# Kernel optimization log

Hardware: AMD Instinct MI355X
Metric: run time of the kernel (lower is better)

## Reference

```python
import jax, jax.numpy as jnp
import numpy as np

B, N = 1, 1024
VOCAB = 32000
DIM = 512
DEPTH = 2
HEADS = 8
DIM_HEAD = 64
DIM_INNER = HEADS * DIM_HEAD      # 512
DIM_FF = 4 * DIM                  # 2048
MAX_SEQ = 1024
EPS = 1e-12


def sq_dist(x, w):
    # squared L2 distance between rows of x [..., d] and rows of w [m, d] -> [..., m]
    xs = jnp.sum(x * x, axis=-1, keepdims=True)
    ws = jnp.sum(w * w, axis=-1)
    return xs - 2.0 * jnp.einsum('...d,md->...m', x, w) + ws


def cdist(x, w):
    # euclidean distance (torch.cdist equivalent)
    return jnp.sqrt(jnp.maximum(sq_dist(x, w), 0.0))


def rmsnorm(x, gamma):
    # F.normalize(x, dim=-1) * sqrt(dim) * (gamma + 1)
    n = jnp.linalg.norm(x, axis=-1, keepdims=True)
    return x / jnp.maximum(n, EPS) * (DIM ** 0.5) * (gamma + 1.0)


def attention(x, qkv_w, out_w):
    b, n, _ = x.shape
    qkv = cdist(x, qkv_w)                                   # [b, n, 3*inner] (to_qkv: squared=False)
    qkv = qkv.reshape(b, n, 3, HEADS, DIM_HEAD)
    qkv = qkv.transpose(2, 0, 3, 1, 4)                      # [3, b, h, n, d]
    q, k, v = qkv[0], qkv[1], qkv[2]
    qs = jnp.sum(q * q, axis=-1)                            # [b, h, n]
    ks = jnp.sum(k * k, axis=-1)                            # [b, h, n]
    # -||q_i - k_j||^2 = 2 q.k - ||q||^2 - ||k||^2
    sim = (2.0 * jnp.einsum('bhid,bhjd->bhij', q, k)
           - qs[..., :, None] - ks[..., None, :]) * (DIM_HEAD ** -0.5)
    attn = jax.nn.softmax(sim, axis=-1)
    o = jnp.einsum('bhij,bhjd->bhid', attn, v)
    o = o.transpose(0, 2, 1, 3).reshape(b, n, DIM_INNER)    # merge heads
    return o @ out_w.T                                      # plain Linear, no bias


def feedforward(x, w_in, b_in, w_out):
    h = -sq_dist(x, w_in) + b_in                            # proj_in: squared=True, negate=True, bias
    h = jax.nn.gelu(h, approximate=False)
    return h @ w_out.T                                      # plain Linear, no bias


def setup_inputs() -> dict:
    key = jax.random.key(0)
    ks = jax.random.split(key, 12)
    nrm = lambda k, s: jax.random.normal(k, s, dtype=jnp.float32)
    return {
        'tokens': jax.random.randint(ks[0], (B, N), 0, VOCAB),
        'token_emb': nrm(ks[1], (VOCAB, DIM)),
        'pos_emb': nrm(ks[2], (MAX_SEQ, DIM)),
        'qkv_w': nrm(ks[3], (DEPTH, 3 * DIM_INNER, DIM)),
        'attn_out_w': nrm(ks[4], (DEPTH, DIM, DIM_INNER)) * 0.02,
        'ff_in_w': nrm(ks[5], (DEPTH, DIM_FF, DIM)),
        'ff_in_b': nrm(ks[6], (DEPTH, DIM_FF)),
        'ff_out_w': nrm(ks[7], (DEPTH, DIM, DIM_FF)) * 0.02,
        'attn_gamma': jnp.zeros((DEPTH, DIM), jnp.float32),
        'ff_gamma': jnp.zeros((DEPTH, DIM), jnp.float32),
        'final_gamma': jnp.zeros((DIM,), jnp.float32),
    }


def reference(tokens, token_emb, pos_emb, qkv_w, attn_out_w, ff_in_w, ff_in_b,
              ff_out_w, attn_gamma, ff_gamma, final_gamma):
    n = tokens.shape[-1]
    x = token_emb[tokens] + pos_emb[:n]                     # [b, n, dim]
    for l in range(DEPTH):
        x = attention(rmsnorm(x, attn_gamma[l]), qkv_w[l], attn_out_w[l]) + x
        x = feedforward(rmsnorm(x, ff_gamma[l]), ff_in_w[l], ff_in_b[l], ff_out_w[l]) + x
    x = rmsnorm(x, final_gamma)
    return -sq_dist(x, token_emb)                           # [b, n, vocab] logits
```

## Files before the change

kernel.cpp:

```cpp
#include <hip/hip_runtime.h>
#include <math.h>

#define DIMM  512
#define NSEQ  1024
#define NHEAD 8
#define DH    64
#define DFF   2048
#define NVOC  32000
#define NDEPTH 2
#define VCENTER 32.0f
#define KVB   64
#define QBLK  32
#define QKOFF ((size_t)NHEAD * NSEQ * DH)
#define FLASH_BLOCKS (NSEQ / QBLK * NHEAD)
#define CONV_ROWS_PER_LAYER (NVOC / NDEPTH)
#define CONV_BLOCKS (CONV_ROWS_PER_LAYER / 64)
#define WCONV_PER_LAYER (3 * DIMM + DIMM + DFF + DIMM)

typedef __attribute__((ext_vector_type(8))) __bf16 bf16x8;
typedef __attribute__((ext_vector_type(4))) __bf16 bf16x4;
typedef __attribute__((ext_vector_type(4))) float f32x4;

__device__ __forceinline__ void g2l16(const void* g, void* l) {
    __builtin_amdgcn_global_load_lds(
        (const __attribute__((address_space(1))) void*)g,
        (__attribute__((address_space(3))) void*)l, 16, 0, 0);
}

#define WAITV(N) asm volatile("s_waitcnt vmcnt(" #N ")" ::: "memory")

template<int NTHR>
__device__ __forceinline__ void conv_weight_row(
    int bid, int l,
    const float* __restrict__ qkv_w, const float* __restrict__ attn_out_w,
    const float* __restrict__ ff_in_w, const float* __restrict__ ff_out_w,
    __bf16* __restrict__ wq16, __bf16* __restrict__ wa16,
    __bf16* __restrict__ wfi16, __bf16* __restrict__ wfo16,
    float* __restrict__ wsq_qkv, float* __restrict__ wsq_ff, float* red) {
    const int tid = threadIdx.x;
    const float* src; __bf16* dst; float* ssq; int K = DIMM; int row;
    if (bid < 3 * DIMM) {
        row = l * 3 * DIMM + bid; src = qkv_w; dst = wq16; ssq = wsq_qkv;
    } else if ((bid -= 3 * DIMM) < DIMM) {
        row = l * DIMM + bid; src = attn_out_w; dst = wa16; ssq = nullptr;
    } else if ((bid -= DIMM) < DFF) {
        row = l * DFF + bid; src = ff_in_w; dst = wfi16; ssq = wsq_ff;
    } else {
        bid -= DFF; row = l * DIMM + bid; src = ff_out_w; dst = wfo16; ssq = nullptr; K = DFF;
    }
    const float* s = src + (size_t)row * K;
    __bf16* d = dst + (size_t)row * K;
    float ss = 0.f;
    for (int j = tid; j < K; j += NTHR) {
        float v = s[j];
        d[j] = (__bf16)v;
        ss += v * v;
    }
    #pragma unroll
    for (int off = 32; off; off >>= 1) ss += __shfl_down(ss, off, 64);
    if ((tid & 63) == 0) red[tid >> 6] = ss;
    __syncthreads();
    if (tid == 0 && ssq) {
        float t = red[0] + red[1];
        if (NTHR == 256) t += red[2] + red[3];
        ssq[row] = t;
    }
}

__launch_bounds__(256)
__global__ void conv_embed(const float* __restrict__ qkv_w, const float* __restrict__ attn_out_w,
                           const float* __restrict__ ff_in_w, const float* __restrict__ ff_out_w,
                           __bf16* __restrict__ wq16, __bf16* __restrict__ wa16,
                           __bf16* __restrict__ wfi16, __bf16* __restrict__ wfo16,
                           float* __restrict__ wsq_qkv, float* __restrict__ wsq_ff,
                           const int* __restrict__ tokens, const float* __restrict__ temb,
                           const float* __restrict__ pemb, const float* __restrict__ gamma,
                           float* __restrict__ x, __bf16* __restrict__ y,
                           float* __restrict__ xs) {
    const int tid = threadIdx.x;
    __shared__ float red[4];

    if (blockIdx.x >= WCONV_PER_LAYER) {
        const int i = blockIdx.x - WCONV_PER_LAYER;
        int tok = tokens[i];
        const float* e = temb + (size_t)tok * DIMM;
        const float* pp = pemb + (size_t)i * DIMM;
        float v0 = e[tid] + pp[tid];
        float v1 = e[tid + 256] + pp[tid + 256];
        x[(size_t)i * DIMM + tid]       = v0;
        x[(size_t)i * DIMM + tid + 256] = v1;
        float ss = v0 * v0 + v1 * v1;
        #pragma unroll
        for (int off = 32; off; off >>= 1) ss += __shfl_down(ss, off, 64);
        if ((tid & 63) == 0) red[tid >> 6] = ss;
        __syncthreads();
        float tot = red[0] + red[1] + red[2] + red[3];
        float scale = 22.627416997969522f / fmaxf(sqrtf(tot), 1e-12f);
        float y0 = v0 * scale * (gamma[tid] + 1.0f);
        float y1 = v1 * scale * (gamma[tid + 256] + 1.0f);
        y[(size_t)i * DIMM + tid]       = (__bf16)y0;
        y[(size_t)i * DIMM + tid + 256] = (__bf16)y1;
        float s2 = y0 * y0 + y1 * y1;
        __syncthreads();
        #pragma unroll
        for (int off = 32; off; off >>= 1) s2 += __shfl_down(s2, off, 64);
        if ((tid & 63) == 0) red[tid >> 6] = s2;
        __syncthreads();
        if (tid == 0) xs[i] = red[0] + red[1] + red[2] + red[3];
        return;
    }

    conv_weight_row<256>(blockIdx.x, 0, qkv_w, attn_out_w, ff_in_w, ff_out_w,
                         wq16, wa16, wfi16, wfo16, wsq_qkv, wsq_ff, red);
}

template<int S>
__launch_bounds__(256)
__global__ void rms_red(const float* __restrict__ parts, float* __restrict__ x,
                        const float* __restrict__ gamma,
                        __bf16* __restrict__ y, float* __restrict__ xs) {
    int i = blockIdx.x;
    int tid = threadIdx.x;
    float* xr = x + (size_t)i * DIMM;
    float v0 = xr[tid], v1 = xr[tid + 256];
    #pragma unroll
    for (int s = 0; s < S; s++) {
        const float* pr = parts + (size_t)s * NSEQ * DIMM + (size_t)i * DIMM;
        v0 += pr[tid];
        v1 += pr[tid + 256];
    }
    xr[tid] = v0;
    xr[tid + 256] = v1;
    float ss = v0 * v0 + v1 * v1;
    __shared__ float red[4];
    #pragma unroll
    for (int off = 32; off; off >>= 1) ss += __shfl_down(ss, off, 64);
    if ((tid & 63) == 0) red[tid >> 6] = ss;
    __syncthreads();
    float tot = red[0] + red[1] + red[2] + red[3];
    float scale = 22.627416997969522f / fmaxf(sqrtf(tot), 1e-12f);
    float y0 = v0 * scale * (gamma[tid] + 1.0f);
    float y1 = v1 * scale * (gamma[tid + 256] + 1.0f);
    y[(size_t)i * DIMM + tid]       = (__bf16)y0;
    y[(size_t)i * DIMM + tid + 256] = (__bf16)y1;
    float s2 = y0 * y0 + y1 * y1;
    __syncthreads();
    #pragma unroll
    for (int off = 32; off; off >>= 1) s2 += __shfl_down(s2, off, 64);
    if ((tid & 63) == 0) red[tid >> 6] = s2;
    __syncthreads();
    if (tid == 0) xs[i] = red[0] + red[1] + red[2] + red[3];
}

enum { MODE_LINEAR = 0, MODE_CDIST = 1, MODE_FFGELU = 2, MODE_LOGITS = 3 };

template<int MODE>
__device__ __forceinline__ void write_elem(void* Cout, int r, int c, int M, float dot,
                                           float xsr, const float* __restrict__ ws,
                                           const float* __restrict__ bias) {
    if (MODE == MODE_LINEAR) {
        ((float*)Cout)[(size_t)r * M + c] = dot;
    } else if (MODE == MODE_FFGELU) {
        float d2 = xsr + ws[c] - 2.0f * dot;
        float hh = -d2 + bias[c];
        float v = 0.5f * hh * (1.0f + erff(hh * 0.70710678118654752f));
        ((__bf16*)Cout)[(size_t)r * M + c] = (__bf16)v;
    }
}

__launch_bounds__(512)
__global__ void gemm_logits(const __bf16* __restrict__ A, const __bf16* __restrict__ W,
                            const float* __restrict__ xs, const float* __restrict__ ws,
                            float* __restrict__ out) {
    __shared__ __align__(16) char smem[49152 + 98304];
    __bf16* As = (__bf16*)smem;
    __bf16* Bs = (__bf16*)(smem + 49152);
    float* tile = (float*)smem;
    const int tid = threadIdx.x;
    const int lane = tid & 63;
    const int wv = tid >> 6;
    const int wr = wv >> 2, wc = wv & 3;

    int id = blockIdx.x;
    id = (id & 7) * 125 + (id >> 3);
    const int row0 = (id & 7) * 128;
    const int col0 = (id >> 3) * 256;

    const int scol = ((tid & 3) ^ ((tid >> 3) & 3)) * 8;
    const __bf16* gA = A + (size_t)(row0 + (tid >> 2)) * DIMM + scol;
    const __bf16* gB = W + (size_t)(col0 + (tid >> 2)) * DIMM + scol;
    const int lrow = lane & 15;
    const int l4 = lane >> 4;
    const int slot = (l4 ^ ((lrow >> 1) & 3)) * 8;

    auto stageChunk = [&](int k0, int b) {
        g2l16(gA + k0,                      As + b * 4096 + tid * 8);
        g2l16(gB + k0,                      Bs + b * 8192 + tid * 8);
        g2l16(gB + (size_t)128 * DIMM + k0, Bs + b * 8192 + 4096 + tid * 8);
    };

    f32x4 acc[4][4] = {};
    const int nP = DIMM >> 6;
    stageChunk(0, 0);  stageChunk(32, 1);
    stageChunk(64, 2); stageChunk(96, 3);
    int pb = 0;
    for (int p = 0; p < nP; p++) {
        if (p < nP - 1) WAITV(6); else WAITV(0);
        __builtin_amdgcn_s_barrier();
        __builtin_amdgcn_sched_barrier(0);
        if (p + 2 < nP) {
            int nb = pb + 2; if (nb >= 3) nb -= 3;
            stageChunk((p + 2) << 6,        nb * 2);
            stageChunk(((p + 2) << 6) + 32, nb * 2 + 1);
        }
        #pragma unroll
        for (int half = 0; half < 2; half++) {
            const int b = pb * 2 + half;
            bf16x8 af[4], bfr[4];
            #pragma unroll
            for (int m = 0; m < 4; m++)
                af[m] = *(const bf16x8*)(As + b * 4096 + (wr * 64 + m * 16 + lrow) * 32 + slot);
            #pragma unroll
            for (int n = 0; n < 4; n++)
                bfr[n] = *(const bf16x8*)(Bs + b * 8192 + (wc * 64 + n * 16 + lrow) * 32 + slot);
            #pragma unroll
            for (int m = 0; m < 4; m++)
                #pragma unroll
                for (int n = 0; n < 4; n++)
                    acc[m][n] = __builtin_amdgcn_mfma_f32_16x16x32_bf16(af[m], bfr[n], acc[m][n], 0, 0, 0);
        }
        if (++pb == 3) pb = 0;
    }
    __syncthreads();

    #pragma unroll
    for (int m = 0; m < 4; m++)
        #pragma unroll
        for (int j = 0; j < 4; j++) {
            const int rl = wr * 64 + m * 16 + l4 * 4 + j;
            const float xsr = xs[row0 + rl];
            const int sw = ((rl >> 2) & 3) << 2;
            #pragma unroll
            for (int n = 0; n < 4; n++) {
                const int cl = wc * 64 + n * 16 + lrow;
                tile[rl * 256 + (cl ^ sw)] = -(xsr + ws[col0 + cl] - 2.0f * acc[m][n][j]);
            }
        }
    __syncthreads();

    #pragma unroll
    for (int jj = 0; jj < 16; jj++) {
        const int f = jj * 2048 + tid * 4;
        const int rr = f >> 8, cc = f & 255;
        const int sw = ((rr >> 2) & 3) << 2;
        f32x4 v = *(const f32x4*)&tile[rr * 256 + (cc ^ sw)];
        __builtin_nontemporal_store(v, (f32x4*)&out[(size_t)(row0 + rr) * NVOC + col0 + cc]);
    }
}

template<int MODE>
__launch_bounds__(256)
__global__ void gemm64(const __bf16* __restrict__ A, const __bf16* __restrict__ W,
                       const float* __restrict__ xs, const float* __restrict__ ws,
                       const float* __restrict__ bias,
                       void* __restrict__ Cout, int K, int Kstr, int M,
                       float* __restrict__ ksout) {
    __shared__ __align__(16) __bf16 As[6 * 64 * 32];
    __shared__ __align__(16) __bf16 Bs[6 * 64 * 32];
    __shared__ float ksred[2][64];
    const int tid = threadIdx.x;
    const int lane = tid & 63;
    const int wv = tid >> 6;
    const int wr = wv >> 1, wc = wv & 1;

    const int gx = gridDim.x;
    const int total = gx * gridDim.y;
    int id = blockIdx.y * gx + blockIdx.x;
    id = (id & 7) * (total >> 3) + (id >> 3);
    const int bx = id % gx;
    const int by = id / gx;
    const int row0 = by * 64;
    const int col0 = bx * 64;
    const size_t zoff = (size_t)blockIdx.z * K;
    float* Cz = (float*)Cout + (size_t)blockIdx.z * NSEQ * M;

    const int scol = (((tid & 3) ^ ((tid >> 3) & 3))) * 8;
    const __bf16* gA = A + (size_t)(row0 + (tid >> 2)) * Kstr + scol + zoff;
    const __bf16* gB = W + (size_t)(col0 + (tid >> 2)) * Kstr + scol + zoff;
    const int lrow = lane & 15;
    const int l4 = lane >> 4;
    const int slot = (l4 ^ ((lrow >> 1) & 3)) * 8;

    auto stageChunk = [&](int k0, int b) {
        g2l16(gA + k0, &As[b * 2048 + tid * 8]);
        g2l16(gB + k0, &Bs[b * 2048 + tid * 8]);
    };

    f32x4 acc[2][2] = {};
    const int nP = K >> 6;
    stageChunk(0, 0);  stageChunk(32, 1);
    stageChunk(64, 2); stageChunk(96, 3);
    int pb = 0;
    for (int p = 0; p < nP; p++) {
        if (p < nP - 1) WAITV(4); else WAITV(0);
        __builtin_amdgcn_s_barrier();
        __builtin_amdgcn_sched_barrier(0);
        if (p + 2 < nP) {
            int nb = pb + 2; if (nb >= 3) nb -= 3;
            stageChunk((p + 2) << 6,        nb * 2);
            stageChunk(((p + 2) << 6) + 32, nb * 2 + 1);
        }
        #pragma unroll
        for (int half = 0; half < 2; half++) {
            const int b = pb * 2 + half;
            bf16x8 af[2], bfr[2];
            #pragma unroll
            for (int m = 0; m < 2; m++)
                af[m] = *(const bf16x8*)&As[b * 2048 + (wr * 32 + m * 16 + lrow) * 32 + slot];
            #pragma unroll
            for (int n = 0; n < 2; n++)
                bfr[n] = *(const bf16x8*)&Bs[b * 2048 + (wc * 32 + n * 16 + lrow) * 32 + slot];
            #pragma unroll
            for (int m = 0; m < 2; m++)
                #pragma unroll
                for (int n = 0; n < 2; n++)
                    acc[m][n] = __builtin_amdgcn_mfma_f32_16x16x32_bf16(af[m], bfr[n], acc[m][n], 0, 0, 0);
        }
        if (++pb == 3) pb = 0;
    }

    const int r_base = row0 + wr * 32 + (lane >> 4) * 4;
    const int c_base = col0 + wc * 32 + (lane & 15);

    if (MODE == MODE_CDIST) {
        const int sec = col0 >> 9;
        const int h = (col0 >> 6) & 7;
        __bf16* Qc = (__bf16*)Cout;
        float pk[2][4];
        #pragma unroll
        for (int m = 0; m < 2; m++)
            #pragma unroll
            for (int j = 0; j < 4; j++) {
                const int r = r_base + m * 16 + j;
                const float xsr = xs[r];
                pk[m][j] = 0.f;
                #pragma unroll
                for (int n = 0; n < 2; n++) {
                    const int c = c_base + n * 16;
                    float d2 = xsr + ws[c] - 2.0f * acc[m][n][j];
                    float v = sqrtf(fmaxf(d2, 0.0f)) - VCENTER;
                    __bf16 bv = (__bf16)v;
                    const int d = c & 63;
                    if (sec == 0)      Qc[((size_t)h * NSEQ + r) * DH + d] = bv;
                    else if (sec == 1) Qc[QKOFF + ((size_t)h * NSEQ + r) * DH + d] = bv;
                    else               Qc[2 * QKOFF + ((size_t)h * DH + d) * NSEQ + r] = bv;
                    float fv = (float)bv;
                    pk[m][j] += fv * fv;
                }
            }
        if (sec == 1) {
            #pragma unroll
            for (int m = 0; m < 2; m++)
                #pragma unroll
                for (int j = 0; j < 4; j++) {
                    float v = pk[m][j];
                    #pragma unroll
                    for (int off = 1; off < 16; off <<= 1) v += __shfl_xor(v, off, 64);
                    if (lrow == 0) ksred[wc][wr * 32 + m * 16 + l4 * 4 + j] = v;
                }
            __syncthreads();
            if (tid < 64)
                ksout[(size_t)h * NSEQ + row0 + tid] = ksred[0][tid] + ksred[1][tid];
        }
    } else {
        #pragma unroll
        for (int m = 0; m < 2; m++)
            #pragma unroll
            for (int j = 0; j < 4; j++) {
                const int r = r_base + m * 16 + j;
                const float xsr = (MODE == MODE_LINEAR) ? 0.f : xs[r];
                #pragma unroll
                for (int n = 0; n < 2; n++)
                    write_elem<MODE>(Cz, r, c_base + n * 16, M, acc[m][n][j], xsr, ws, bias);
            }
    }
}

__launch_bounds__(128)
__global__ void flash_attn(const __bf16* __restrict__ Qc, const __bf16* __restrict__ Kc,
                           const __bf16* __restrict__ VcT, const float* __restrict__ ks,
                           __bf16* __restrict__ O,
                           const float* __restrict__ temb, __bf16* __restrict__ temb16,
                           float* __restrict__ wsq_temb, int conv_row0,
                           const float* __restrict__ qkv_w, const float* __restrict__ attn_out_w,
                           const float* __restrict__ ff_in_w, const float* __restrict__ ff_out_w,
                           __bf16* __restrict__ wq16, __bf16* __restrict__ wa16,
                           __bf16* __restrict__ wfi16, __bf16* __restrict__ wfo16,
                           float* __restrict__ wsq_qkv, float* __restrict__ wsq_ff) {
    const int tid = threadIdx.x, lane = tid & 63, wv = tid >> 6;

    if (blockIdx.x >= FLASH_BLOCKS + CONV_BLOCKS) {
        __shared__ float redc[2];
        conv_weight_row<128>(blockIdx.x - FLASH_BLOCKS - CONV_BLOCKS, 1,
                             qkv_w, attn_out_w, ff_in_w, ff_out_w,
                             wq16, wa16, wfi16, wfo16, wsq_qkv, wsq_ff, redc);
        return;
    }
    if (blockIdx.x >= FLASH_BLOCKS) {
        const int base = conv_row0 + (blockIdx.x - FLASH_BLOCKS) * 64;
        for (int it = 0; it < 32; it++) {
            const int row = base + it * 2 + wv;
            const float* src = temb + (size_t)row * DIMM;
            float4 a = ((const float4*)src)[lane];
            float4 b2 = ((const float4*)src)[lane + 64];
            float ss = a.x * a.x + a.y * a.y + a.z * a.z + a.w * a.w
                     + b2.x * b2.x + b2.y * b2.y + b2.z * b2.z + b2.w * b2.w;
            bf16x4 oa, ob;
            oa.x = (__bf16)a.x;  oa.y = (__bf16)a.y;  oa.z = (__bf16)a.z;  oa.w = (__bf16)a.w;
            ob.x = (__bf16)b2.x; ob.y = (__bf16)b2.y; ob.z = (__bf16)b2.z; ob.w = (__bf16)b2.w;
            *(bf16x4*)&temb16[(size_t)row * DIMM + lane * 4]       = oa;
            *(bf16x4*)&temb16[(size_t)row * DIMM + 256 + lane * 4] = ob;
            #pragma unroll
            for (int off = 32; off; off >>= 1) ss += __shfl_down(ss, off, 64);
            if (lane == 0) wsq_temb[row] = ss;
        }
        return;
    }

    __shared__ __align__(16) __bf16 Qs[QBLK * 64];
    __shared__ __align__(16) __bf16 Ks[2][64 * 64];
    __shared__ __align__(16) __bf16 Vs[2][64 * 64];
    __shared__ __align__(16) __bf16 Ps[2][16 * 64];
    __shared__ float kss[2][64];
    const int h = blockIdx.x >> 5, q0 = (blockIdx.x & 31) * QBLK;
    const int l15 = lane & 15, l4 = lane >> 4;

    #pragma unroll
    for (int pass = 0; pass < 2; pass++) {
        int gl = tid + pass * 128, r = gl >> 3, gs = (gl & 7) ^ (r & 7);
        g2l16(Qc + ((size_t)h * NSEQ + q0 + r) * DH + gs * 8, &Qs[gl * 8]);
    }
    auto stage = [&](int c, int buf) {
        const int kv0 = c * KVB;
        #pragma unroll
        for (int pass = 0; pass < 4; pass++) {
            int gl = tid + pass * 128, r = gl >> 3, gs = (gl & 7) ^ (r & 7);
            g2l16(Kc + ((size_t)h * NSEQ + kv0 + r) * DH + gs * 8, &Ks[buf][gl * 8]);
            g2l16(VcT + ((size_t)h * DH + r) * NSEQ + kv0 + gs * 8, &Vs[buf][gl * 8]);
        }
        if (tid < KVB) kss[buf][tid] = ks[(size_t)h * NSEQ + c * KVB + tid];
    };
    stage(0, 0);
    __syncthreads();

    bf16x8 qf[2];
    #pragma unroll
    for (int s = 0; s < 2; s++) {
        int row = wv * 16 + l15;
        int g = (l4 + 4 * s) ^ (row & 7);
        qf[s] = *(const bf16x8*)&Qs[row * 64 + g * 8];
    }

    float m_j[4], l_j[4];
    f32x4 o_[4] = {};
    #pragma unroll
    for (int j = 0; j < 4; j++) { m_j[j] = -1e30f; l_j[j] = 0.f; }

    for (int c = 0; c < NSEQ / KVB; c++) {
        const int b = c & 1;
        if (c + 1 < NSEQ / KVB) stage(c + 1, b ^ 1);

        f32x4 sa[4] = {};
        #pragma unroll
        for (int s = 0; s < 2; s++) {
            bf16x8 kf[4];
            #pragma unroll
            for (int n = 0; n < 4; n++) {
                int row = n * 16 + l15;
                int g = (l4 + 4 * s) ^ (row & 7);
                kf[n] = *(const bf16x8*)&Ks[b][row * 64 + g * 8];
            }
            #pragma unroll
            for (int n = 0; n < 4; n++)
                sa[n] = __builtin_amdgcn_mfma_f32_16x16x32_bf16(qf[s], kf[n], sa[n], 0, 0, 0);
        }
        float ksv[4];
        #pragma unroll
        for (int n = 0; n < 4; n++) ksv[n] = kss[b][n * 16 + l15];

        float scale[4];
        #pragma unroll
        for (int j = 0; j < 4; j++) {
            float mx = -1e30f;
            #pragma unroll
            for (int n = 0; n < 4; n++) {
                float sv = sa[n][j] * 0.25f - ksv[n] * 0.125f;
                sa[n][j] = sv;
                mx = fmaxf(mx, sv);
            }
            #pragma unroll
            for (int off = 1; off < 16; off <<= 1) mx = fmaxf(mx, __shfl_xor(mx, off, 64));
            float mn = fmaxf(m_j[j], mx);
            scale[j] = expf(m_j[j] - mn);
            m_j[j] = mn;
        }
        #pragma unroll
        for (int j = 0; j < 4; j++) {
            const int row = l4 * 4 + j;
            float ls = 0.f;
            #pragma unroll
            for (int n = 0; n < 4; n++) {
                float pv = expf(sa[n][j] - m_j[j]);
                ls += pv;
                int col = n * 16 + l15;
                Ps[wv][row * 64 + ((((col >> 3) ^ (row & 7)) << 3) | (col & 7))] = (__bf16)pv;
            }
            #pragma unroll
            for (int off = 1; off < 16; off <<= 1) ls += __shfl_xor(ls, off, 64);
            l_j[j] = l_j[j] * scale[j] + ls;
            o_[0][j] *= scale[j]; o_[1][j] *= scale[j];
            o_[2][j] *= scale[j]; o_[3][j] *= scale[j];
        }

        #pragma unroll
        for (int s = 0; s < 2; s++) {
            int g = (l4 + 4 * s) ^ (l15 & 7);
            bf16x8 pf = *(const bf16x8*)&Ps[wv][l15 * 64 + g * 8];
            #pragma unroll
            for (int n = 0; n < 4; n++) {
                int row = n * 16 + l15;
                int gv = (l4 + 4 * s) ^ (row & 7);
                bf16x8 vf = *(const bf16x8*)&Vs[b][row * 64 + gv * 8];
                o_[n] = __builtin_amdgcn_mfma_f32_16x16x32_bf16(pf, vf, o_[n], 0, 0, 0);
            }
        }
        __syncthreads();
    }

    #pragma unroll
    for (int n = 0; n < 4; n++)
        #pragma unroll
        for (int j = 0; j < 4; j++) {
            int row = q0 + wv * 16 + l4 * 4 + j;
            int d = n * 16 + l15;
            O[(size_t)row * DIMM + h * DH + d] = (__bf16)(o_[n][j] / l_j[j] + VCENTER);
        }
}

extern "C" void kernel_launch(void* const* d_in, const int* in_sizes, int n_in,
                              void* d_out, int out_size, void* d_ws, size_t ws_size,
                              hipStream_t stream) {
    (void)in_sizes; (void)n_in; (void)out_size; (void)ws_size;
    const int*   tokens      = (const int*)d_in[0];
    const float* temb        = (const float*)d_in[1];
    const float* pemb        = (const float*)d_in[2];
    const float* qkv_w       = (const float*)d_in[3];
    const float* attn_out_w  = (const float*)d_in[4];
    const float* ff_in_w     = (const float*)d_in[5];
    const float* ff_in_b     = (const float*)d_in[6];
    const float* ff_out_w    = (const float*)d_in[7];
    const float* attn_gamma  = (const float*)d_in[8];
    const float* ff_gamma    = (const float*)d_in[9];
    const float* final_gamma = (const float*)d_in[10];
    float* out = (float*)d_out;

    char* p = (char*)d_ws;
    float*  x        = (float*)p;  p += (size_t)NSEQ * DIMM * 4;
    float*  xs       = (float*)p;  p += (size_t)NSEQ * 4;
    float*  wsq_qkv  = (float*)p;  p += (size_t)NDEPTH * 3 * DIMM * 4;
    float*  wsq_ff   = (float*)p;  p += (size_t)NDEPTH * DFF * 4;
    float*  wsq_temb = (float*)p;  p += (size_t)NVOC * 4;
    float*  ksbuf    = (float*)p;  p += (size_t)NHEAD * NSEQ * 4;
    float*  parts    = (float*)p;  p += (size_t)4 * NSEQ * DIMM * 4;
    __bf16* y16      = (__bf16*)p; p += (size_t)NSEQ * DIMM * 2;
    __bf16* o16      = (__bf16*)p; p += (size_t)NSEQ * DIMM * 2;
    __bf16* Qc       = (__bf16*)p; p += 3 * QKOFF * 2;
    __bf16* hb16     = (__bf16*)p; p += (size_t)NSEQ * DFF * 2;
    __bf16* wq16     = (__bf16*)p; p += (size_t)NDEPTH * 3 * DIMM * DIMM * 2;
    __bf16* wa16     = (__bf16*)p; p += (size_t)NDEPTH * DIMM * DIMM * 2;
    __bf16* wfi16    = (__bf16*)p; p += (size_t)NDEPTH * DFF * DIMM * 2;
    __bf16* wfo16    = (__bf16*)p; p += (size_t)NDEPTH * DIMM * DFF * 2;
    __bf16* temb16   = (__bf16*)p; p += (size_t)NVOC * DIMM * 2;
    __bf16* Kc  = Qc + QKOFF;
    __bf16* VcT = Qc + 2 * QKOFF;

    conv_embed<<<WCONV_PER_LAYER + NSEQ, 256, 0, stream>>>(
        qkv_w, attn_out_w, ff_in_w, ff_out_w,
        wq16, wa16, wfi16, wfo16, wsq_qkv, wsq_ff,
        tokens, temb, pemb, attn_gamma, x, y16, xs);

    for (int l = 0; l < NDEPTH; l++) {
        const __bf16* qkvw = wq16  + (size_t)l * 3 * DIMM * DIMM;
        const __bf16* aow  = wa16  + (size_t)l * DIMM * DIMM;
        const __bf16* fiw  = wfi16 + (size_t)l * DFF * DIMM;
        const __bf16* fow  = wfo16 + (size_t)l * DIMM * DFF;
        const float*  fib  = ff_in_b + (size_t)l * DFF;
        const float*  next_gamma = (l + 1 < NDEPTH) ? (attn_gamma + (l + 1) * DIMM)
                                                    : final_gamma;

        gemm64<MODE_CDIST><<<dim3(3 * DIMM / 64, NSEQ / 64), 256, 0, stream>>>(
            y16, qkvw, xs, wsq_qkv + l * 3 * DIMM, nullptr, Qc, DIMM, DIMM, 3 * DIMM, ksbuf);
        const int flashGrid = FLASH_BLOCKS + CONV_BLOCKS + ((l == 0) ? WCONV_PER_LAYER : 0);
        flash_attn<<<flashGrid, 128, 0, stream>>>(
            Qc, Kc, VcT, ksbuf, o16, temb, temb16, wsq_temb, l * CONV_ROWS_PER_LAYER,
            qkv_w, attn_out_w, ff_in_w, ff_out_w,
            wq16, wa16, wfi16, wfo16, wsq_qkv, wsq_ff);
        gemm64<MODE_LINEAR><<<dim3(DIMM / 64, NSEQ / 64, 2), 256, 0, stream>>>(
            o16, aow, nullptr, nullptr, nullptr, parts, DIMM / 2, DIMM, DIMM, nullptr);
        rms_red<2><<<NSEQ, 256, 0, stream>>>(parts, x, ff_gamma + l * DIMM, y16, xs);

        gemm64<MODE_FFGELU><<<dim3(DFF / 64, NSEQ / 64), 256, 0, stream>>>(
            y16, fiw, xs, wsq_ff + l * DFF, fib, hb16, DIMM, DIMM, DFF, nullptr);
        gemm64<MODE_LINEAR><<<dim3(DIMM / 64, NSEQ / 64, 4), 256, 0, stream>>>(
            hb16, fow, nullptr, nullptr, nullptr, parts, DFF / 4, DFF, DIMM, nullptr);
        rms_red<4><<<NSEQ, 256, 0, stream>>>(parts, x, next_gamma, y16, xs);
    }

    gemm_logits<<<1000, 512, 0, stream>>>(y16, temb16, xs, wsq_temb, out);
}
```

Before: 220.4 us.

## Use single-wave flash attention blocks with vmcnt-based double buffering

Flash attention blocks drop from two waves (32 query rows) to one wave (16 query rows), which doubles the grid. Because each block is a single wavefront, __syncthreads can be replaced by s_waitcnt vmcnt on the global-to-LDS loads. Prefetch now runs two KV tiles ahead and the ks load goes through a 4-byte direct-to-LDS transfer. The side conversion work is reshaped for 64 threads. This improves occupancy and removes barriers, but each KV tile is now loaded twice as often in total, and correctness depends on exact vmcnt counts (17) matching the number of issued loads.

```diff
diff --git a/kernel.cpp b/kernel.cpp
--- a/kernel.cpp
+++ b/kernel.cpp
@@ -10,7 +10,7 @@
 #define NDEPTH 2
 #define VCENTER 32.0f
 #define KVB   64
-#define QBLK  32
+#define QBLK  16
 #define QKOFF ((size_t)NHEAD * NSEQ * DH)
 #define FLASH_BLOCKS (NSEQ / QBLK * NHEAD)
 #define CONV_ROWS_PER_LAYER (NVOC / NDEPTH)
@@ -25,6 +25,11 @@
     __builtin_amdgcn_global_load_lds(
         (const __attribute__((address_space(1))) void*)g,
         (__attribute__((address_space(3))) void*)l, 16, 0, 0);
+}
+__device__ __forceinline__ void g2l4(const void* g, void* l) {
+    __builtin_amdgcn_global_load_lds(
+        (const __attribute__((address_space(1))) void*)g,
+        (__attribute__((address_space(3))) void*)l, 4, 0, 0);
 }
 
 #define WAITV(N) asm volatile("s_waitcnt vmcnt(" #N ")" ::: "memory")
@@ -58,12 +63,16 @@
     }
     #pragma unroll
     for (int off = 32; off; off >>= 1) ss += __shfl_down(ss, off, 64);
-    if ((tid & 63) == 0) red[tid >> 6] = ss;
-    __syncthreads();
-    if (tid == 0 && ssq) {
-        float t = red[0] + red[1];
-        if (NTHR == 256) t += red[2] + red[3];
-        ssq[row] = t;
+    if (NTHR == 64) {
+        if (tid == 0 && ssq) ssq[row] = ss;
+    } else {
+        if ((tid & 63) == 0) red[tid >> 6] = ss;
+        __syncthreads();
+        if (tid == 0 && ssq) {
+            float t = red[0] + red[1];
+            if (NTHR == 256) t += red[2] + red[3];
+            ssq[row] = t;
+        }
     }
 }
 
@@ -386,7 +395,7 @@
     }
 }
 
-__launch_bounds__(128)
+__launch_bounds__(64)
 __global__ void flash_attn(const __bf16* __restrict__ Qc, const __bf16* __restrict__ Kc,
                            const __bf16* __restrict__ VcT, const float* __restrict__ ks,
                            __bf16* __restrict__ O,
@@ -397,19 +406,18 @@
                            __bf16* __restrict__ wq16, __bf16* __restrict__ wa16,
                            __bf16* __restrict__ wfi16, __bf16* __restrict__ wfo16,
                            float* __restrict__ wsq_qkv, float* __restrict__ wsq_ff) {
-    const int tid = threadIdx.x, lane = tid & 63, wv = tid >> 6;
+    const int tid = threadIdx.x, lane = tid;
 
     if (blockIdx.x >= FLASH_BLOCKS + CONV_BLOCKS) {
-        __shared__ float redc[2];
-        conv_weight_row<128>(blockIdx.x - FLASH_BLOCKS - CONV_BLOCKS, 1,
-                             qkv_w, attn_out_w, ff_in_w, ff_out_w,
-                             wq16, wa16, wfi16, wfo16, wsq_qkv, wsq_ff, redc);
+        conv_weight_row<64>(blockIdx.x - FLASH_BLOCKS - CONV_BLOCKS, 1,
+                            qkv_w, attn_out_w, ff_in_w, ff_out_w,
+                            wq16, wa16, wfi16, wfo16, wsq_qkv, wsq_ff, nullptr);
         return;
     }
     if (blockIdx.x >= FLASH_BLOCKS) {
         const int base = conv_row0 + (blockIdx.x - FLASH_BLOCKS) * 64;
-        for (int it = 0; it < 32; it++) {
-            const int row = base + it * 2 + wv;
+        for (int it = 0; it < 64; it++) {
+            const int row = base + it;
             const float* src = temb + (size_t)row * DIMM;
             float4 a = ((const float4*)src)[lane];
             float4 b2 = ((const float4*)src)[lane + 64];
@@ -430,33 +438,34 @@
     __shared__ __align__(16) __bf16 Qs[QBLK * 64];
     __shared__ __align__(16) __bf16 Ks[2][64 * 64];
     __shared__ __align__(16) __bf16 Vs[2][64 * 64];
-    __shared__ __align__(16) __bf16 Ps[2][16 * 64];
+    __shared__ __align__(16) __bf16 Ps[16 * 64];
     __shared__ float kss[2][64];
-    const int h = blockIdx.x >> 5, q0 = (blockIdx.x & 31) * QBLK;
+    const int h = blockIdx.x >> 6, q0 = (blockIdx.x & 63) * QBLK;
     const int l15 = lane & 15, l4 = lane >> 4;
 
     #pragma unroll
     for (int pass = 0; pass < 2; pass++) {
-        int gl = tid + pass * 128, r = gl >> 3, gs = (gl & 7) ^ (r & 7);
+        int gl = tid + pass * 64, r = gl >> 3, gs = (gl & 7) ^ (r & 7);
         g2l16(Qc + ((size_t)h * NSEQ + q0 + r) * DH + gs * 8, &Qs[gl * 8]);
     }
     auto stage = [&](int c, int buf) {
         const int kv0 = c * KVB;
         #pragma unroll
-        for (int pass = 0; pass < 4; pass++) {
-            int gl = tid + pass * 128, r = gl >> 3, gs = (gl & 7) ^ (r & 7);
+        for (int pass = 0; pass < 8; pass++) {
+            int gl = tid + pass * 64, r = gl >> 3, gs = (gl & 7) ^ (r & 7);
             g2l16(Kc + ((size_t)h * NSEQ + kv0 + r) * DH + gs * 8, &Ks[buf][gl * 8]);
             g2l16(VcT + ((size_t)h * DH + r) * NSEQ + kv0 + gs * 8, &Vs[buf][gl * 8]);
         }
-        if (tid < KVB) kss[buf][tid] = ks[(size_t)h * NSEQ + c * KVB + tid];
+        g2l4(ks + (size_t)h * NSEQ + kv0, &kss[buf][0]);
     };
     stage(0, 0);
-    __syncthreads();
+    stage(1, 1);
+    WAITV(17);
 
     bf16x8 qf[2];
     #pragma unroll
     for (int s = 0; s < 2; s++) {
-        int row = wv * 16 + l15;
+        int row = l15;
         int g = (l4 + 4 * s) ^ (row & 7);
         qf[s] = *(const bf16x8*)&Qs[row * 64 + g * 8];
     }
@@ -468,7 +477,7 @@
 
     for (int c = 0; c < NSEQ / KVB; c++) {
         const int b = c & 1;
-        if (c + 1 < NSEQ / KVB) stage(c + 1, b ^ 1);
+        if (c > 0) { if (c < NSEQ / KVB - 1) WAITV(17); else WAITV(0); }
 
         f32x4 sa[4] = {};
         #pragma unroll
@@ -513,7 +522,7 @@
                 float pv = expf(sa[n][j] - m_j[j]);
                 ls += pv;
                 int col = n * 16 + l15;
-                Ps[wv][row * 64 + ((((col >> 3) ^ (row & 7)) << 3) | (col & 7))] = (__bf16)pv;
+                Ps[row * 64 + ((((col >> 3) ^ (row & 7)) << 3) | (col & 7))] = (__bf16)pv;
             }
             #pragma unroll
             for (int off = 1; off < 16; off <<= 1) ls += __shfl_xor(ls, off, 64);
@@ -525,7 +534,7 @@
         #pragma unroll
         for (int s = 0; s < 2; s++) {
             int g = (l4 + 4 * s) ^ (l15 & 7);
-            bf16x8 pf = *(const bf16x8*)&Ps[wv][l15 * 64 + g * 8];
+            bf16x8 pf = *(const bf16x8*)&Ps[l15 * 64 + g * 8];
             #pragma unroll
             for (int n = 0; n < 4; n++) {
                 int row = n * 16 + l15;
@@ -534,14 +543,18 @@
                 o_[n] = __builtin_amdgcn_mfma_f32_16x16x32_bf16(pf, vf, o_[n], 0, 0, 0);
             }
         }
-        __syncthreads();
+
+        if (c + 2 < NSEQ / KVB) {
+            __builtin_amdgcn_sched_barrier(0);
+            stage(c + 2, b);
+        }
     }
 
     #pragma unroll
     for (int n = 0; n < 4; n++)
         #pragma unroll
         for (int j = 0; j < 4; j++) {
-            int row = q0 + wv * 16 + l4 * 4 + j;
+            int row = q0 + l4 * 4 + j;
             int d = n * 16 + l15;
             O[(size_t)row * DIMM + h * DH + d] = (__bf16)(o_[n][j] / l_j[j] + VCENTER);
         }
@@ -601,7 +614,7 @@
         gemm64<MODE_CDIST><<<dim3(3 * DIMM / 64, NSEQ / 64), 256, 0, stream>>>(
             y16, qkvw, xs, wsq_qkv + l * 3 * DIMM, nullptr, Qc, DIMM, DIMM, 3 * DIMM, ksbuf);
         const int flashGrid = FLASH_BLOCKS + CONV_BLOCKS + ((l == 0) ? WCONV_PER_LAYER : 0);
-        flash_attn<<<flashGrid, 128, 0, stream>>>(
+        flash_attn<<<flashGrid, 64, 0, stream>>>(
             Qc, Kc, VcT, ksbuf, o16, temb, temb16, wsq_temb, l * CONV_ROWS_PER_LAYER,
             qkv_w, attn_out_w, ff_in_w, ff_out_w,
             wq16, wa16, wfi16, wfo16, wsq_qkv, wsq_ff);
```

Result: slower. 233.2 us (+5.8%).
